# Kernel tuning notes

Hardware: AMD Instinct MI355X
Metric: run time of the kernel (lower is better)

The kernel has to match this reference:

```python
import jax, jax.numpy as jnp
import numpy as np

B, T, D, H = 4, 2048, 1024, 16
HD = D // H

def setup_inputs() -> dict:
    key = jax.random.key(0)
    ks = jax.random.split(key, 7)
    s = 1.0 / np.sqrt(D)
    return {
        "x": jax.random.normal(ks[0], (B, T, D), dtype=jnp.float32),
        "w_qkv": jax.random.uniform(ks[1], (D, 3 * D), jnp.float32, -s, s),
        "b_qkv": jax.random.uniform(ks[2], (3 * D,), jnp.float32, -s, s),
        "w_proj": jax.random.uniform(ks[3], (D, D), jnp.float32, -s, s),
        "b_proj": jax.random.uniform(ks[4], (D,), jnp.float32, -s, s),
        "ln_gamma": jnp.ones((D,), jnp.float32),
        "ln_beta": jnp.zeros((D,), jnp.float32),
    }

def reference(x, w_qkv, b_qkv, w_proj, b_proj, ln_gamma, ln_beta):
    eps = 1e-5
    scale = HD ** -0.5
    residual = x
    # Pre-norm LayerNorm over last dim
    mu = jnp.mean(x, axis=-1, keepdims=True)
    var = jnp.mean(jnp.square(x - mu), axis=-1, keepdims=True)
    xn = (x - mu) * jax.lax.rsqrt(var + eps) * ln_gamma + ln_beta
    # QKV projection: (B,T,3D) -> (3,B,H,T,HD)
    qkv = xn @ w_qkv + b_qkv
    qkv = qkv.reshape(B, T, 3, H, HD).transpose(2, 0, 3, 1, 4)
    q, k, v = qkv[0], qkv[1], qkv[2]
    # Scaled dot-product attention (full T x T scores, as in source)
    attn = jnp.einsum('bhqd,bhkd->bhqk', q, k) * scale
    attn = jax.nn.softmax(attn, axis=-1)
    out = jnp.einsum('bhqk,bhkd->bhqd', attn, v)
    out = out.transpose(0, 2, 1, 3).reshape(B, T, D)
    out = out @ w_proj + b_proj
    return residual + out
```

## Files before the change

kernel.cpp:

```cpp
#include <hip/hip_runtime.h>
#include <cstdint>
#include <cstddef>

#define B_ 4
#define T_ 2048
#define D_ 1024
#define H_ 16

typedef __attribute__((ext_vector_type(8))) short short8;
typedef __attribute__((ext_vector_type(4))) float f32x4;
typedef __attribute__((ext_vector_type(8))) unsigned short u16x8;

__device__ __forceinline__ unsigned short f2b16(float f) {
  union { float f; unsigned int u; } un; un.f = f;
  unsigned int r = un.u + 0x7fffu + ((un.u >> 16) & 1u);
  return (unsigned short)(r >> 16);
}
__device__ __forceinline__ void async_cp16(const void* g, void* l) {
  __builtin_amdgcn_global_load_lds((const __attribute__((address_space(1))) void*)g,
                                   (__attribute__((address_space(3))) void*)l,
                                   16, 0, 0);
}

__global__ __launch_bounds__(256) void ln_kernel(const float* __restrict__ x,
                                                 const float* __restrict__ gamma,
                                                 const float* __restrict__ beta,
                                                 unsigned short* __restrict__ xn) {
  const int row = blockIdx.x;
  const int t = threadIdx.x;
  const float4 v = ((const float4*)(x + (size_t)row * D_))[t];
  float s  = v.x + v.y + v.z + v.w;
  float s2 = v.x*v.x + v.y*v.y + v.z*v.z + v.w*v.w;
  #pragma unroll
  for (int off = 32; off > 0; off >>= 1) {
    s  += __shfl_down(s, off);
    s2 += __shfl_down(s2, off);
  }
  __shared__ float sh[8];
  const int wv = t >> 6, lane = t & 63;
  if (lane == 0) { sh[wv] = s; sh[4 + wv] = s2; }
  __syncthreads();
  if (t == 0) {
    float ts  = sh[0] + sh[1] + sh[2] + sh[3];
    float ts2 = sh[4] + sh[5] + sh[6] + sh[7];
    float mu  = ts * (1.0f / D_);
    float var = ts2 * (1.0f / D_) - mu * mu;
    sh[0] = mu;
    sh[1] = rsqrtf(var + 1e-5f);
  }
  __syncthreads();
  const float mu = sh[0], rs = sh[1];
  const float4 g  = ((const float4*)gamma)[t];
  const float4 bb = ((const float4*)beta)[t];
  ushort4 o;
  o.x = f2b16((v.x - mu) * rs * g.x + bb.x);
  o.y = f2b16((v.y - mu) * rs * g.y + bb.y);
  o.z = f2b16((v.z - mu) * rs * g.z + bb.z);
  o.w = f2b16((v.w - mu) * rs * g.w + bb.w);
  ((ushort4*)(xn + (size_t)row * D_))[t] = o;
}

__global__ __launch_bounds__(256) void transpose_cast(const float* __restrict__ w,
                                                      unsigned short* __restrict__ wT,
                                                      int K, int N) {
  __shared__ float tile[32][33];
  const int n0 = blockIdx.x * 32;
  const int k0 = blockIdx.y * 32;
  const int tx = threadIdx.x, ty = threadIdx.y;
  #pragma unroll
  for (int i = 0; i < 32; i += 8)
    tile[ty + i][tx] = w[(size_t)(k0 + ty + i) * N + n0 + tx];
  __syncthreads();
  #pragma unroll
  for (int i = 0; i < 32; i += 8)
    wT[(size_t)(n0 + ty + i) * K + k0 + tx] = f2b16(tile[tx][ty + i]);
}

__global__ __launch_bounds__(256) void transpose_v(const unsigned short* __restrict__ vB,
                                                   unsigned short* __restrict__ vtB) {
  __shared__ unsigned short tile[64 * 66];
  const int tid = threadIdx.x;
  const int bh = blockIdx.x;
  const int t0 = blockIdx.y * 64;
  const int lr = tid >> 2, lc = (tid & 3) * 16;
  const unsigned short* src = vB + ((size_t)bh * T_ + t0) * 64;
  *(u16x8*)&tile[lr * 66 + lc]     = *(const u16x8*)(src + (size_t)lr * 64 + lc);
  *(u16x8*)&tile[lr * 66 + lc + 8] = *(const u16x8*)(src + (size_t)lr * 64 + lc + 8);
  __syncthreads();
  const int dv = tid >> 2, cb = (tid & 3) * 16;
  unsigned short outv[16];
  #pragma unroll
  for (int j = 0; j < 16; ++j) {
    const int c = cb + j;
    const int t = (c & 32) | ((c & 4) << 2) | ((c & 16) >> 1) | ((c & 8) >> 1) | (c & 3);
    outv[j] = tile[t * 66 + dv];
  }
  unsigned short* dst = vtB + ((size_t)bh * 64 + dv) * T_ + t0 + cb;
  *(u16x8*)dst       = *(const u16x8*)&outv[0];
  *(u16x8*)(dst + 8) = *(const u16x8*)&outv[8];
}

template <int MODE>
__global__ __launch_bounds__(256) void gemm_bt(const unsigned short* __restrict__ A,
                                               const unsigned short* __restrict__ Bt,
                                               const float* __restrict__ bias,
                                               const float* __restrict__ resid,
                                               unsigned short* __restrict__ qB,
                                               unsigned short* __restrict__ kB,
                                               unsigned short* __restrict__ vB,
                                               float* __restrict__ outF,
                                               int M, int N, int K) {
  __shared__ unsigned short As[128 * 32];
  __shared__ unsigned short Bs[128 * 32];
  const int tid  = threadIdx.x;
  const int lane = tid & 63;
  const int wv   = tid >> 6;
  const int wm   = (wv & 1) * 64;
  const int wn   = (wv >> 1) * 64;
  const int tileM = blockIdx.x * 128;
  const int tileN = blockIdx.y * 128;
  const int l15 = lane & 15, quad = lane >> 4;
  const int sRow = tid >> 2;
  const int sCol = (tid & 3) * 8;

  f32x4 acc[4][4] = {};

  const unsigned short* aG0 = A  + (size_t)(tileM + sRow) * K + sCol;
  const unsigned short* aG1 = A  + (size_t)(tileM + 64 + sRow) * K + sCol;
  const unsigned short* bG0 = Bt + (size_t)(tileN + sRow) * K + sCol;
  const unsigned short* bG1 = Bt + (size_t)(tileN + 64 + sRow) * K + sCol;
  unsigned short* lA0 = &As[tid * 8];
  unsigned short* lA1 = &As[2048 + tid * 8];
  unsigned short* lB0 = &Bs[tid * 8];
  unsigned short* lB1 = &Bs[2048 + tid * 8];

  for (int k0 = 0; k0 < K; k0 += 32) {
    async_cp16(aG0 + k0, lA0);
    async_cp16(aG1 + k0, lA1);
    async_cp16(bG0 + k0, lB0);
    async_cp16(bG1 + k0, lB1);
    __syncthreads();

    short8 a[4], b[4];
    #pragma unroll
    for (int i = 0; i < 4; ++i) {
      a[i] = *(const short8*)&As[(wm + i * 16 + l15) * 32 + quad * 8];
      b[i] = *(const short8*)&Bs[(wn + i * 16 + l15) * 32 + quad * 8];
    }
    #pragma unroll
    for (int mi = 0; mi < 4; ++mi)
      #pragma unroll
      for (int ni = 0; ni < 4; ++ni)
        acc[mi][ni] = __builtin_amdgcn_mfma_f32_16x16x32_bf16(a[mi], b[ni], acc[mi][ni], 0, 0, 0);
    __syncthreads();
  }

  if constexpr (MODE == 1) {
    #pragma unroll
    for (int ni = 0; ni < 4; ++ni) {
      const int col = tileN + wn + ni * 16 + l15;
      const float bv = bias[col];
      #pragma unroll
      for (int mi = 0; mi < 4; ++mi) {
        #pragma unroll
        for (int r = 0; r < 4; ++r) {
          const int row = tileM + wm + mi * 16 + quad * 4 + r;
          const size_t idx = (size_t)row * N + col;
          outF[idx] = acc[mi][ni][r] + bv + resid[idx];
        }
      }
    }
  } else {
    __shared__ unsigned short Es[4][64 * 72];
    unsigned short* E = Es[wv];
    const int colBase = tileN + wn;
    #pragma unroll
    for (int ni = 0; ni < 4; ++ni) {
      const int col = colBase + ni * 16 + l15;
      const float bv = bias[col];
      const float sc = (col < 1024) ? 0.180336880f : 1.0f;
      #pragma unroll
      for (int mi = 0; mi < 4; ++mi)
        #pragma unroll
        for (int r = 0; r < 4; ++r)
          E[(mi * 16 + quad * 4 + r) * 72 + ni * 16 + l15] =
              f2b16((acc[mi][ni][r] + bv) * sc);
    }
    const int sec = colBase >> 10;
    const int hh  = (colBase & 1023) >> 6;
    unsigned short* outSec = (sec == 0) ? qB : (sec == 1) ? kB : vB;
    #pragma unroll
    for (int it = 0; it < 8; ++it) {
      const int lrow = it * 8 + (lane >> 3);
      const int row = tileM + wm + lrow;
      const int b_ = row >> 11, t = row & 2047;
      const u16x8 val = *(const u16x8*)&E[lrow * 72 + (lane & 7) * 8];
      *(u16x8*)(outSec + ((size_t)(b_ * 16 + hh) * T_ + t) * 64 + (lane & 7) * 8) = val;
    }
  }
}

__global__ __launch_bounds__(256, 4) void attn_mfma(const unsigned short* __restrict__ qB,
                                                    const unsigned short* __restrict__ kB,
                                                    const unsigned short* __restrict__ vtB,
                                                    unsigned short* __restrict__ aout) {
  __shared__ unsigned short Ks[2][64 * 64];
  __shared__ unsigned short Vs[2][64 * 64];

  const int tid = threadIdx.x;
  const int bid = blockIdx.x;
  const int bh = bid & 63;
  const int qb = bid >> 6;
  const int b = bh >> 4, h = bh & 15;
  const int wv = tid >> 6, lane = tid & 63;
  const int l15 = lane & 15, quad = lane >> 4;

  const unsigned short* qP = qB  + (size_t)bh * T_ * 64;
  const unsigned short* kP = kB  + (size_t)bh * T_ * 64;
  const unsigned short* vP = vtB + (size_t)bh * 64 * T_;
  const int q0 = qb * 128 + wv * 32;

  short8 qf[2][2];
  #pragma unroll
  for (int mi = 0; mi < 2; ++mi)
    #pragma unroll
    for (int ks = 0; ks < 2; ++ks)
      qf[mi][ks] = *(const short8*)(qP + ((size_t)(q0 + mi * 16 + l15)) * 64 + ks * 32 + quad * 8);

  const short8 onesf = {0x3F80, 0x3F80, 0x3F80, 0x3F80, 0x3F80, 0x3F80, 0x3F80, 0x3F80};
  f32x4 accO[2][5] = {};

  const int lrow  = lane >> 3;
  const int lchnk = (lane & 7) ^ (lrow & 7);
  const size_t kOff0 = (size_t)((wv * 2 + 0) * 8 + lrow) * 64 + lchnk * 8;
  const size_t kOff1 = (size_t)((wv * 2 + 1) * 8 + lrow) * 64 + lchnk * 8;
  const size_t vOff0 = (size_t)((wv * 2 + 0) * 8 + lrow) * T_ + lchnk * 8;
  const size_t vOff1 = (size_t)((wv * 2 + 1) * 8 + lrow) * T_ + lchnk * 8;
  const int lOff0 = (wv * 2 + 0) * 512 + lane * 8;
  const int lOff1 = (wv * 2 + 1) * 512 + lane * 8;

  async_cp16(kP + kOff0, &Ks[0][lOff0]);
  async_cp16(kP + kOff1, &Ks[0][lOff1]);
  async_cp16(vP + vOff0, &Vs[0][lOff0]);
  async_cp16(vP + vOff1, &Vs[0][lOff1]);
  __syncthreads();

  for (int kt = 0; kt < 32; ++kt) {
    const int buf = kt & 1;
    if (kt + 1 < 32) {
      const unsigned short* kg = kP + (size_t)(kt + 1) * 64 * 64;
      const unsigned short* vg = vP + (kt + 1) * 64;
      async_cp16(kg + kOff0, &Ks[buf ^ 1][lOff0]);
      async_cp16(kg + kOff1, &Ks[buf ^ 1][lOff1]);
      async_cp16(vg + vOff0, &Vs[buf ^ 1][lOff0]);
      async_cp16(vg + vOff1, &Vs[buf ^ 1][lOff1]);
    }
    const unsigned short* K_ = Ks[buf];
    const unsigned short* V_ = Vs[buf];

    f32x4 accT[4][2] = {};
    #pragma unroll
    for (int ks = 0; ks < 2; ++ks) {
      #pragma unroll
      for (int cc = 0; cc < 4; ++cc) {
        const short8 kb = *(const short8*)&K_[(cc * 16 + l15) * 64 +
                                              (((ks << 2) | quad) ^ (l15 & 7)) * 8];
        accT[cc][0] = __builtin_amdgcn_mfma_f32_16x16x32_bf16(kb, qf[0][ks], accT[cc][0], 0, 0, 0);
        accT[cc][1] = __builtin_amdgcn_mfma_f32_16x16x32_bf16(kb, qf[1][ks], accT[cc][1], 0, 0, 0);
      }
    }

    short8 pa[2][2];
    #pragma unroll
    for (int mi = 0; mi < 2; ++mi) {
      #pragma unroll
      for (int ks = 0; ks < 2; ++ks) {
        union { unsigned short u[8]; short8 s; } pk;
        #pragma unroll
        for (int r = 0; r < 4; ++r) {
          union { float f; unsigned int u; } e0, e1;
          e0.f = __builtin_amdgcn_exp2f(accT[2 * ks + 0][mi][r]);
          e1.f = __builtin_amdgcn_exp2f(accT[2 * ks + 1][mi][r]);
          pk.u[r]     = (unsigned short)(e0.u >> 16);
          pk.u[4 + r] = (unsigned short)(e1.u >> 16);
        }
        pa[mi][ks] = pk.s;
      }
    }

    #pragma unroll
    for (int ks = 0; ks < 2; ++ks) {
      short8 vb[4];
      #pragma unroll
      for (int nj = 0; nj < 4; ++nj)
        vb[nj] = *(const short8*)&V_[(nj * 16 + l15) * 64 +
                                     (((ks << 2) | quad) ^ (l15 & 7)) * 8];
      #pragma unroll
      for (int mi = 0; mi < 2; ++mi) {
        #pragma unroll
        for (int nj = 0; nj < 4; ++nj)
          accO[mi][nj] = __builtin_amdgcn_mfma_f32_16x16x32_bf16(pa[mi][ks], vb[nj], accO[mi][nj], 0, 0, 0);
        accO[mi][4] = __builtin_amdgcn_mfma_f32_16x16x32_bf16(pa[mi][ks], onesf, accO[mi][4], 0, 0, 0);
      }
    }

    __syncthreads();
  }

  #pragma unroll
  for (int mi = 0; mi < 2; ++mi) {
    #pragma unroll
    for (int r = 0; r < 4; ++r) {
      const float inv = 1.0f / accO[mi][4][r];
      const int row = q0 + mi * 16 + quad * 4 + r;
      unsigned short* op = aout + (size_t)(b * T_ + row) * D_ + h * 64 + l15;
      #pragma unroll
      for (int nj = 0; nj < 4; ++nj)
        op[nj * 16] = f2b16(accO[mi][nj][r] * inv);
    }
  }
}

extern "C" void kernel_launch(void* const* d_in, const int* in_sizes, int n_in,
                              void* d_out, int out_size, void* d_ws, size_t ws_size,
                              hipStream_t stream) {
  const float* x      = (const float*)d_in[0];
  const float* w_qkv  = (const float*)d_in[1];
  const float* b_qkv  = (const float*)d_in[2];
  const float* w_proj = (const float*)d_in[3];
  const float* b_proj = (const float*)d_in[4];
  const float* ln_g   = (const float*)d_in[5];
  const float* ln_b   = (const float*)d_in[6];
  float* out = (float*)d_out;

  char* ws = (char*)d_ws;
  unsigned short* xn   = (unsigned short*)(ws);
  unsigned short* wTq  = (unsigned short*)(ws + (size_t)(16 << 20));
  unsigned short* wTp  = (unsigned short*)(ws + (size_t)(22 << 20));
  unsigned short* qBuf = (unsigned short*)(ws + (size_t)(24 << 20));
  unsigned short* kBuf = (unsigned short*)(ws + (size_t)(40 << 20));
  unsigned short* vBuf = (unsigned short*)(ws + (size_t)(56 << 20));
  unsigned short* vtB  = (unsigned short*)(ws + (size_t)(72 << 20));
  unsigned short* aout = xn;

  ln_kernel<<<8192, 256, 0, stream>>>(x, ln_g, ln_b, xn);
  transpose_cast<<<dim3(96, 32), dim3(32, 8), 0, stream>>>(w_qkv, wTq, 1024, 3072);
  transpose_cast<<<dim3(32, 32), dim3(32, 8), 0, stream>>>(w_proj, wTp, 1024, 1024);
  gemm_bt<0><<<dim3(64, 24), 256, 0, stream>>>(xn, wTq, b_qkv, nullptr,
                                               qBuf, kBuf, vBuf, nullptr, 8192, 3072, 1024);
  transpose_v<<<dim3(64, 32), 256, 0, stream>>>(vBuf, vtB);
  attn_mfma<<<1024, 256, 0, stream>>>(qBuf, kBuf, vtB, aout);
  gemm_bt<1><<<dim3(64, 8), 256, 0, stream>>>(aout, wTp, b_proj, x,
                                              nullptr, nullptr, nullptr, out, 8192, 1024, 1024);
}
```

Before: 279.6 us.

## Replace QKV GEMM with 256x256-tile double-buffered pipelined MFMA kernel

Adds a dedicated QKV projection kernel using 256x256 output tiles, 512 threads, BK=64 with XOR-swizzled LDS, double-buffered async global-to-LDS loads interleaved with MFMA quadrants, priority hints, and a block-index remap for L2 locality. It aims to raise arithmetic intensity and overlap loads with compute compared with the old 128x128 single-stage GEMM. The generic gemm_bt is reduced to the projection epilogue only. Large LDS use (128KB) limits occupancy, and the hand-written waitcnt and barrier sequencing risks subtle race bugs.

```diff
diff --git a/kernel.cpp b/kernel.cpp
--- a/kernel.cpp
+++ b/kernel.cpp
@@ -100,14 +100,178 @@
   *(u16x8*)(dst + 8) = *(const u16x8*)&outv[8];
 }
 
+__global__ __launch_bounds__(512, 2) void gemm256_qkv(const unsigned short* __restrict__ A,
+                                                      const unsigned short* __restrict__ Bt,
+                                                      const float* __restrict__ bias,
+                                                      unsigned short* __restrict__ qB,
+                                                      unsigned short* __restrict__ kB,
+                                                      unsigned short* __restrict__ vB) {
+  constexpr int K = 1024;
+  constexpr int NT = K / 64;
+  __shared__ __align__(16) unsigned short As[32768];
+  __shared__ __align__(16) unsigned short Bs[32768];
+
+  const int tid  = threadIdx.x;
+  const int lane = tid & 63;
+  const int wv   = tid >> 6;
+  const int l15  = lane & 15, quad = lane >> 4;
+  const int wr   = wv >> 1;
+  const int wc   = wv & 1;
+
+  const int w = (blockIdx.x & 7) * 48 + (blockIdx.x >> 3);
+  const int tileM = (w & 31) * 256;
+  const int tileN = (w >> 5) * 256;
+
+  const int sr  = tid >> 3;
+  const int scs = ((tid & 7) ^ (sr & 7)) * 8;
+  const unsigned short* gA = A  + (size_t)(tileM + sr) * K + scs;
+  const unsigned short* gB = Bt + (size_t)(tileN + sr) * K + scs;
+
+  auto stageA = [&](int h, int ko, int wbuf) {
+    const unsigned short* g = gA + (size_t)(h * 128) * K + ko;
+    unsigned short* l = &As[wbuf * 16384 + h * 8192 + tid * 8];
+    async_cp16(g, l);
+    async_cp16(g + (size_t)64 * K, l + 4096);
+  };
+  auto stageB = [&](int h, int ko, int wbuf) {
+    const unsigned short* g = gB + (size_t)(h * 128) * K + ko;
+    unsigned short* l = &Bs[wbuf * 16384 + h * 8192 + tid * 8];
+    async_cp16(g, l);
+    async_cp16(g + (size_t)64 * K, l + 4096);
+  };
+
+  const int rA  = wr * 32 + l15;
+  const int rB  = wc * 64 + l15;
+  const int ck0 = ((0 + quad) ^ (l15 & 7)) * 8;
+  const int ck1 = ((4 + quad) ^ (l15 & 7)) * 8;
+
+  f32x4 acc[2][2][2][4] = {};
+
+#define MFMA16(QM, QN, AF, BF)                                                          \
+  do {                                                                                  \
+    _Pragma("unroll") for (int fm = 0; fm < 2; ++fm)                                    \
+    _Pragma("unroll") for (int fn = 0; fn < 4; ++fn) {                                  \
+      acc[QM][QN][fm][fn] = __builtin_amdgcn_mfma_f32_16x16x32_bf16(                    \
+          AF[fm][0], BF[fn][0], acc[QM][QN][fm][fn], 0, 0, 0);                          \
+      acc[QM][QN][fm][fn] = __builtin_amdgcn_mfma_f32_16x16x32_bf16(                    \
+          AF[fm][1], BF[fn][1], acc[QM][QN][fm][fn], 0, 0, 0);                          \
+    }                                                                                   \
+  } while (0)
+
+  stageA(0, 0, 0);
+  stageB(0, 0, 0);
+  stageB(1, 0, 0);
+  stageA(1, 0, 0);
+  asm volatile("s_waitcnt vmcnt(4)" ::: "memory");
+  asm volatile("s_barrier" ::: "memory");
+
+  #pragma unroll 2
+  for (int kt = 0; kt < NT; ++kt) {
+    const int buf = kt & 1;
+    const unsigned short* Ab = &As[buf * 16384];
+    const unsigned short* Bb = &Bs[buf * 16384];
+    const int wbuf = buf ^ 1;
+    const bool st = (kt + 1) < NT;
+    const int ko = (kt + 1) * 64;
+
+    short8 a[2][2], b0[4][2], b1[4][2];
+
+    #pragma unroll
+    for (int fm = 0; fm < 2; ++fm) {
+      a[fm][0] = *(const short8*)&Ab[(rA + fm * 16) * 64 + ck0];
+      a[fm][1] = *(const short8*)&Ab[(rA + fm * 16) * 64 + ck1];
+    }
+    #pragma unroll
+    for (int fn = 0; fn < 4; ++fn) {
+      b0[fn][0] = *(const short8*)&Bb[(rB + fn * 16) * 64 + ck0];
+      b0[fn][1] = *(const short8*)&Bb[(rB + fn * 16) * 64 + ck1];
+    }
+    if (st) stageA(0, ko, wbuf);
+    asm volatile("s_waitcnt lgkmcnt(0)" ::: "memory");
+    __builtin_amdgcn_sched_barrier(0);
+    __builtin_amdgcn_s_setprio(1);
+    MFMA16(0, 0, a, b0);
+    __builtin_amdgcn_s_setprio(0);
+    if (st) asm volatile("s_waitcnt vmcnt(4)" ::: "memory");
+    else    asm volatile("s_waitcnt vmcnt(2)" ::: "memory");
+    asm volatile("s_barrier" ::: "memory");
+
+    #pragma unroll
+    for (int fn = 0; fn < 4; ++fn) {
+      b1[fn][0] = *(const short8*)&Bb[8192 + (rB + fn * 16) * 64 + ck0];
+      b1[fn][1] = *(const short8*)&Bb[8192 + (rB + fn * 16) * 64 + ck1];
+    }
+    if (st) stageB(0, ko, wbuf);
+    asm volatile("s_waitcnt lgkmcnt(0)" ::: "memory");
+    __builtin_amdgcn_sched_barrier(0);
+    __builtin_amdgcn_s_setprio(1);
+    MFMA16(0, 1, a, b1);
+    __builtin_amdgcn_s_setprio(0);
+    if (st) asm volatile("s_waitcnt vmcnt(4)" ::: "memory");
+    else    asm volatile("s_waitcnt vmcnt(0)" ::: "memory");
+    asm volatile("s_barrier" ::: "memory");
+
+    #pragma unroll
+    for (int fm = 0; fm < 2; ++fm) {
+      a[fm][0] = *(const short8*)&Ab[8192 + (rA + fm * 16) * 64 + ck0];
+      a[fm][1] = *(const short8*)&Ab[8192 + (rA + fm * 16) * 64 + ck1];
+    }
+    if (st) stageB(1, ko, wbuf);
+    asm volatile("s_waitcnt lgkmcnt(0)" ::: "memory");
+    __builtin_amdgcn_sched_barrier(0);
+    __builtin_amdgcn_s_setprio(1);
+    MFMA16(1, 0, a, b0);
+    __builtin_amdgcn_s_setprio(0);
+    asm volatile("s_barrier" ::: "memory");
+
+    if (st) stageA(1, ko, wbuf);
+    __builtin_amdgcn_s_setprio(1);
+    MFMA16(1, 1, a, b1);
+    __builtin_amdgcn_s_setprio(0);
+    if (st) asm volatile("s_waitcnt vmcnt(4)" ::: "memory");
+    asm volatile("s_barrier" ::: "memory");
+  }
+#undef MFMA16
+
+  unsigned short* E = &As[wv * 2304];
+  #pragma unroll
+  for (int qm = 0; qm < 2; ++qm) {
+    #pragma unroll
+    for (int qn = 0; qn < 2; ++qn) {
+      const int colBase = tileN + qn * 128 + wc * 64;
+      const int rowBase = tileM + qm * 128 + wr * 32;
+      #pragma unroll
+      for (int fn = 0; fn < 4; ++fn) {
+        const int col = colBase + fn * 16 + l15;
+        const float bv = bias[col];
+        const float sc = (col < 1024) ? 0.180336880f : 1.0f;
+        #pragma unroll
+        for (int fm = 0; fm < 2; ++fm)
+          #pragma unroll
+          for (int r = 0; r < 4; ++r)
+            E[(fm * 16 + quad * 4 + r) * 72 + fn * 16 + l15] =
+                f2b16((acc[qm][qn][fm][fn][r] + bv) * sc);
+      }
+      const int secq = colBase >> 10;
+      const int hh   = (colBase & 1023) >> 6;
+      unsigned short* outSec = (secq == 0) ? qB : (secq == 1) ? kB : vB;
+      #pragma unroll
+      for (int it = 0; it < 4; ++it) {
+        const int lrow = it * 8 + (lane >> 3);
+        const int row = rowBase + lrow;
+        const int b_ = row >> 11, t = row & 2047;
+        const u16x8 val = *(const u16x8*)&E[lrow * 72 + (lane & 7) * 8];
+        *(u16x8*)(outSec + ((size_t)(b_ * 16 + hh) * T_ + t) * 64 + (lane & 7) * 8) = val;
+      }
+    }
+  }
+}
+
 template <int MODE>
 __global__ __launch_bounds__(256) void gemm_bt(const unsigned short* __restrict__ A,
                                                const unsigned short* __restrict__ Bt,
                                                const float* __restrict__ bias,
                                                const float* __restrict__ resid,
-                                               unsigned short* __restrict__ qB,
-                                               unsigned short* __restrict__ kB,
-                                               unsigned short* __restrict__ vB,
                                                float* __restrict__ outF,
                                                int M, int N, int K) {
   __shared__ unsigned short As[128 * 32];
@@ -155,47 +319,18 @@
     __syncthreads();
   }
 
-  if constexpr (MODE == 1) {
-    #pragma unroll
-    for (int ni = 0; ni < 4; ++ni) {
-      const int col = tileN + wn + ni * 16 + l15;
-      const float bv = bias[col];
-      #pragma unroll
-      for (int mi = 0; mi < 4; ++mi) {
-        #pragma unroll
-        for (int r = 0; r < 4; ++r) {
-          const int row = tileM + wm + mi * 16 + quad * 4 + r;
-          const size_t idx = (size_t)row * N + col;
-          outF[idx] = acc[mi][ni][r] + bv + resid[idx];
-        }
-      }
-    }
-  } else {
-    __shared__ unsigned short Es[4][64 * 72];
-    unsigned short* E = Es[wv];
-    const int colBase = tileN + wn;
-    #pragma unroll
-    for (int ni = 0; ni < 4; ++ni) {
-      const int col = colBase + ni * 16 + l15;
-      const float bv = bias[col];
-      const float sc = (col < 1024) ? 0.180336880f : 1.0f;
-      #pragma unroll
-      for (int mi = 0; mi < 4; ++mi)
-        #pragma unroll
-        for (int r = 0; r < 4; ++r)
-          E[(mi * 16 + quad * 4 + r) * 72 + ni * 16 + l15] =
-              f2b16((acc[mi][ni][r] + bv) * sc);
-    }
-    const int sec = colBase >> 10;
-    const int hh  = (colBase & 1023) >> 6;
-    unsigned short* outSec = (sec == 0) ? qB : (sec == 1) ? kB : vB;
-    #pragma unroll
-    for (int it = 0; it < 8; ++it) {
-      const int lrow = it * 8 + (lane >> 3);
-      const int row = tileM + wm + lrow;
-      const int b_ = row >> 11, t = row & 2047;
-      const u16x8 val = *(const u16x8*)&E[lrow * 72 + (lane & 7) * 8];
-      *(u16x8*)(outSec + ((size_t)(b_ * 16 + hh) * T_ + t) * 64 + (lane & 7) * 8) = val;
+  #pragma unroll
+  for (int ni = 0; ni < 4; ++ni) {
+    const int col = tileN + wn + ni * 16 + l15;
+    const float bv = bias[col];
+    #pragma unroll
+    for (int mi = 0; mi < 4; ++mi) {
+      #pragma unroll
+      for (int r = 0; r < 4; ++r) {
+        const int row = tileM + wm + mi * 16 + quad * 4 + r;
+        const size_t idx = (size_t)row * N + col;
+        outF[idx] = acc[mi][ni][r] + bv + resid[idx];
+      }
     }
   }
 }
@@ -346,10 +481,8 @@
   ln_kernel<<<8192, 256, 0, stream>>>(x, ln_g, ln_b, xn);
   transpose_cast<<<dim3(96, 32), dim3(32, 8), 0, stream>>>(w_qkv, wTq, 1024, 3072);
   transpose_cast<<<dim3(32, 32), dim3(32, 8), 0, stream>>>(w_proj, wTp, 1024, 1024);
-  gemm_bt<0><<<dim3(64, 24), 256, 0, stream>>>(xn, wTq, b_qkv, nullptr,
-                                               qBuf, kBuf, vBuf, nullptr, 8192, 3072, 1024);
+  gemm256_qkv<<<384, 512, 0, stream>>>(xn, wTq, b_qkv, qBuf, kBuf, vBuf);
   transpose_v<<<dim3(64, 32), 256, 0, stream>>>(vBuf, vtB);
   attn_mfma<<<1024, 256, 0, stream>>>(qBuf, kBuf, vtB, aout);
-  gemm_bt<1><<<dim3(64, 8), 256, 0, stream>>>(aout, wTp, b_proj, x,
-                                              nullptr, nullptr, nullptr, out, 8192, 1024, 1024);
-}
+  gemm_bt<1><<<dim3(64, 8), 256, 0, stream>>>(aout, wTp, b_proj, x, out, 8192, 1024, 1024);
+}
```

Result: no change. 281.7 us (+0.7%).
